# Performance work log

Hardware: AMD Instinct MI355X
Metric: run time of the kernel (lower is better)

The kernel has to match this reference:

```python
import jax, jax.numpy as jnp
import numpy as np

N_VERTICES = 1_000_000
N_EDGES = 16_000_000


def setup_inputs() -> dict:
    key = jax.random.key(0)
    k1, k2, k3 = jax.random.split(key, 3)
    vertex_attr = jax.random.normal(k1, (N_VERTICES, 2), dtype=jnp.float32)
    edgeij_pair = jax.random.randint(k2, (2, N_EDGES), 0, N_VERTICES, dtype=jnp.int64)
    edge_attr = jax.random.normal(k3, (N_EDGES, 2), dtype=jnp.float32)
    g = jnp.zeros((1, 1), dtype=jnp.float32)
    batch = jnp.zeros((N_VERTICES,), dtype=jnp.int64)
    return {"vertex_attr": vertex_attr, "edgeij_pair": edgeij_pair,
            "edge_attr": edge_attr, "g": g, "batch": batch}


def reference(vertex_attr, edgeij_pair, edge_attr, g, batch):
    # c_ij: second edge feature column, [E, 1]
    c_ij = edge_attr[:, 1:2]
    b_i = vertex_attr[:, 0:1]  # [N, 1]
    x_i = vertex_attr[:, 1:2]  # [N, 1]
    n_vertices = x_i.shape[0]
    # edge-to-vertex aggregation: sum c_ij into receiving vertex i (row 0)
    cbar_i = jax.ops.segment_sum(c_ij, edgeij_pair[0], num_segments=n_vertices)
    r_i = b_i - cbar_i
    return jnp.concatenate([b_i, x_i, r_i], axis=1)  # [N, 3]
```

## Files before the change

kernel.cpp:

```cpp
#include <hip/hip_runtime.h>


#define BSHIFT 11
#define BSIZE (1 << BSHIFT)
#define NBUCK_PAD 512
#define TILE 8192
#define TPB 1024

__global__ __launch_bounds__(TPB, 8)
void vu_partition(const int* __restrict__ src,
                  const float* __restrict__ eattr,
                  unsigned long long* __restrict__ pairs,
                  unsigned int* __restrict__ alloc,
                  int ne, int nbuck, int cap) {
    __shared__ unsigned long long sorted[TILE];
    __shared__ unsigned int hist[NBUCK_PAD];
    __shared__ unsigned int base_l[NBUCK_PAD];
    __shared__ unsigned int cursor[NBUCK_PAD];
    __shared__ unsigned int gbase[NBUCK_PAD];
    __shared__ unsigned int wsum[8];
    __shared__ unsigned int wexcl[8];

    int t = threadIdx.x;
    int tile0 = blockIdx.x * TILE;
    int lim = ne - tile0; if (lim > TILE) lim = TILE;
    bool full = (lim == TILE);

    if (t < NBUCK_PAD) hist[t] = 0u;
    __syncthreads();

    int4 sA, sB;
    float4 cA0, cA1, cB0, cB1;
    if (full) {
        const int4* s4 = (const int4*)(src + tile0);
        sA = s4[t];
        sB = s4[t + TPB];
        const float4* ef = (const float4*)eattr;
        int b0 = (tile0 >> 1) + 2 * t;
        cA0 = ef[b0];
        cA1 = ef[b0 + 1];
        cB0 = ef[b0 + 2048];
        cB1 = ef[b0 + 2049];
        atomicAdd(&hist[((unsigned)sA.x) >> BSHIFT], 1u);
        atomicAdd(&hist[((unsigned)sA.y) >> BSHIFT], 1u);
        atomicAdd(&hist[((unsigned)sA.z) >> BSHIFT], 1u);
        atomicAdd(&hist[((unsigned)sA.w) >> BSHIFT], 1u);
        atomicAdd(&hist[((unsigned)sB.x) >> BSHIFT], 1u);
        atomicAdd(&hist[((unsigned)sB.y) >> BSHIFT], 1u);
        atomicAdd(&hist[((unsigned)sB.z) >> BSHIFT], 1u);
        atomicAdd(&hist[((unsigned)sB.w) >> BSHIFT], 1u);
    } else {
        for (int i = t; i < lim; i += TPB)
            atomicAdd(&hist[((unsigned)src[tile0 + i]) >> BSHIFT], 1u);
    }
    __syncthreads();

    unsigned int mycnt = (t < NBUCK_PAD) ? hist[t] : 0u;
    unsigned int x = mycnt;
    #pragma unroll
    for (int off = 1; off < 64; off <<= 1) {
        unsigned int v = __shfl_up(x, off, 64);
        if ((t & 63) >= off) x += v;
    }
    if (t < NBUCK_PAD && (t & 63) == 63) wsum[t >> 6] = x;
    __syncthreads();
    if (t < 8) {
        unsigned int s = 0u;
        for (int k = 0; k < t; ++k) s += wsum[k];
        wexcl[t] = s;
    }
    __syncthreads();
    if (t < NBUCK_PAD) {
        unsigned int inc = x + wexcl[t >> 6];
        unsigned int excl = inc - mycnt;
        base_l[t] = excl;
        cursor[t] = excl;
        gbase[t] = (t < nbuck && mycnt) ? atomicAdd(&alloc[t], mycnt) : 0u;
    }
    __syncthreads();

#define VU_SCAT(sv, cv) do { \
        unsigned int q_ = ((unsigned)(sv)) >> BSHIFT; \
        unsigned int pos_ = atomicAdd(&cursor[q_], 1u); \
        sorted[pos_] = ((unsigned long long)__float_as_uint(cv) << 32) \
                       | (unsigned)(sv); } while (0)
    if (full) {
        VU_SCAT(sA.x, cA0.y); VU_SCAT(sA.y, cA0.w);
        VU_SCAT(sA.z, cA1.y); VU_SCAT(sA.w, cA1.w);
        VU_SCAT(sB.x, cB0.y); VU_SCAT(sB.y, cB0.w);
        VU_SCAT(sB.z, cB1.y); VU_SCAT(sB.w, cB1.w);
    } else {
        for (int i = t; i < lim; i += TPB) {
            int e = tile0 + i;
            int s = src[e];
            float2 ec = ((const float2*)eattr)[e];
            VU_SCAT(s, ec.y);
        }
    }
#undef VU_SCAT
    __syncthreads();

    for (int i = t; i < lim; i += TPB) {
        unsigned long long p = sorted[i];
        unsigned int q = ((unsigned int)p) >> BSHIFT;
        unsigned int dst = q * (unsigned int)cap + gbase[q]
                         + ((unsigned int)i - base_l[q]);
        unsigned int hi = q * (unsigned int)cap + (unsigned int)cap - 1u;
        if (dst > hi) dst = hi;
        pairs[dst] = p;
    }
}

__global__ __launch_bounds__(1024)
void vu_aggregate(const unsigned long long* __restrict__ pairs,
                  const unsigned int* __restrict__ alloc,
                  const float* __restrict__ vattr,
                  float* __restrict__ out,
                  int nv, int cap) {
    __shared__ float acc[BSIZE];
    __shared__ float obuf[BSIZE * 3];
    int q = blockIdx.x;
    int t = threadIdx.x;
    acc[t] = 0.0f;
    acc[t + 1024] = 0.0f;

    int v0 = q << BSHIFT;
    int iv0 = v0 + t, iv1 = v0 + t + 1024;
    float2 va0 = make_float2(0.f, 0.f), va1 = make_float2(0.f, 0.f);
    if (iv0 < nv) va0 = ((const float2*)vattr)[iv0];
    if (iv1 < nv) va1 = ((const float2*)vattr)[iv1];
    __syncthreads();

    unsigned int cnt = alloc[q];
    if (cnt > (unsigned int)cap) cnt = (unsigned int)cap;
    const unsigned long long* p = pairs + (size_t)q * (size_t)cap;
    const ulonglong2* p2 = (const ulonglong2*)p;
    unsigned int n2 = cnt >> 1;

#define VU_ACC(v64) do { \
        atomicAdd(&acc[((unsigned int)(v64)) & (BSIZE - 1)], \
                  __uint_as_float((unsigned int)((v64) >> 32))); } while (0)

    unsigned int i = t;
    for (; i + 3u * 1024u < n2; i += 4096u) {
        ulonglong2 v0 = p2[i];
        ulonglong2 v1 = p2[i + 1024u];
        ulonglong2 v2 = p2[i + 2048u];
        ulonglong2 v3 = p2[i + 3072u];
        VU_ACC(v0.x); VU_ACC(v0.y);
        VU_ACC(v1.x); VU_ACC(v1.y);
        VU_ACC(v2.x); VU_ACC(v2.y);
        VU_ACC(v3.x); VU_ACC(v3.y);
    }
    for (; i < n2; i += 1024u) {
        ulonglong2 v = p2[i];
        VU_ACC(v.x); VU_ACC(v.y);
    }
    if (t == 0 && (cnt & 1u)) {
        unsigned long long v = p[cnt - 1];
        VU_ACC(v);
    }
#undef VU_ACC
    __syncthreads();

    if (iv0 < nv) {
        obuf[3 * t + 0] = va0.x;
        obuf[3 * t + 1] = va0.y;
        obuf[3 * t + 2] = va0.x - acc[t];
    }
    {
        int i2 = t + 1024;
        if (iv1 < nv) {
            obuf[3 * i2 + 0] = va1.x;
            obuf[3 * i2 + 1] = va1.y;
            obuf[3 * i2 + 2] = va1.x - acc[i2];
        }
    }
    __syncthreads();

    long fbase = (long)q * (BSIZE * 3);
    int nfl = 3 * nv - (int)fbase;
    if (nfl > BSIZE * 3) nfl = BSIZE * 3;
    if (nfl > 0) {
        float4* o4 = (float4*)(out + fbase);
        const float4* s4 = (const float4*)obuf;
        int n4 = nfl >> 2;
        for (int j = t; j < n4; j += 1024) o4[j] = s4[j];
        for (int j = (n4 << 2) + t; j < nfl; j += 1024) out[fbase + j] = obuf[j];
    }
}

__global__ void vu_init_kernel(const float* __restrict__ vattr,
                               float* __restrict__ out, int n) {
    int i = blockIdx.x * blockDim.x + threadIdx.x;
    if (i < n) {
        float2 v = ((const float2*)vattr)[i];
        out[3 * i + 0] = v.x;
        out[3 * i + 1] = v.y;
        out[3 * i + 2] = v.x;
    }
}

__global__ void vu_scatter_kernel(const int* __restrict__ src,
                                  const float* __restrict__ eattr,
                                  float* __restrict__ out, int ne) {
    int t = blockIdx.x * blockDim.x + threadIdx.x;
    int e0 = t * 4;
    if (e0 + 3 < ne) {
        int4 idx = ((const int4*)src)[t];
        float4 a = ((const float4*)eattr)[2 * t + 0];
        float4 b = ((const float4*)eattr)[2 * t + 1];
        atomicAdd(&out[3 * idx.x + 2], -a.y);
        atomicAdd(&out[3 * idx.y + 2], -a.w);
        atomicAdd(&out[3 * idx.z + 2], -b.y);
        atomicAdd(&out[3 * idx.w + 2], -b.w);
    } else {
        for (int e = e0; e < ne; ++e)
            atomicAdd(&out[3 * src[e] + 2], -eattr[2 * e + 1]);
    }
}

extern "C" void kernel_launch(void* const* d_in, const int* in_sizes, int n_in,
                              void* d_out, int out_size, void* d_ws, size_t ws_size,
                              hipStream_t stream) {
    const float* vattr = (const float*)d_in[0];
    const int* edges = (const int*)d_in[1];
    const float* eattr = (const float*)d_in[2];
    float* out = (float*)d_out;

    int nv = in_sizes[0] / 2;
    int ne = in_sizes[2] / 2;

    int nbuck = (nv + BSIZE - 1) >> BSHIFT;
    int mean = ne / nbuck;
    int cap = mean + mean / 8 + 1024;
    cap = (cap + 15) & ~15;

    size_t alloc_bytes = 4096;
    size_t pair_bytes = (size_t)nbuck * (size_t)cap * 8ull;
    size_t need = alloc_bytes + pair_bytes;

    if (ws_size >= need && nbuck <= NBUCK_PAD) {
        unsigned int* alloc = (unsigned int*)d_ws;
        unsigned long long* pairs = (unsigned long long*)((char*)d_ws + alloc_bytes);
        (void)hipMemsetAsync(alloc, 0, (size_t)nbuck * 4, stream);

        int p1_blocks = (ne + TILE - 1) / TILE;
        vu_partition<<<p1_blocks, TPB, 0, stream>>>(edges, eattr, pairs, alloc,
                                                    ne, nbuck, cap);
        vu_aggregate<<<nbuck, 1024, 0, stream>>>(pairs, alloc, vattr, out, nv, cap);
    } else {
        int threads = 256;
        int blocks = (nv + threads - 1) / threads;
        vu_init_kernel<<<blocks, threads, 0, stream>>>(vattr, out, nv);
        int nt = (ne + 3) / 4;
        blocks = (nt + threads - 1) / threads;
        vu_scatter_kernel<<<blocks, threads, 0, stream>>>(edges, eattr, out, ne);
    }
}
```

Before: 390.3 us.

## Make partition kernel persistent with register prefetch of next tile

The partition kernel now runs as a fixed grid of persistent blocks that loop over edge tiles. Each iteration loads the next tile's source indices and edge values into registers before working on the current tile, so global load latency overlaps the LDS histogram, scan and scatter work. A custom barrier waits only on LDS counters, so the outstanding global prefetches are not drained at each barrier. The vector loads become strided scalar loads, and the extra registers could lower occupancy.

```diff
diff --git a/kernel.cpp b/kernel.cpp
--- a/kernel.cpp
+++ b/kernel.cpp
@@ -6,6 +6,11 @@
 #define NBUCK_PAD 512
 #define TILE 8192
 #define TPB 1024
+#define PGRID 512
+
+#define BARL() do { \
+    asm volatile("s_waitcnt lgkmcnt(0)" ::: "memory"); \
+    __builtin_amdgcn_s_barrier(); } while (0)
 
 __global__ __launch_bounds__(TPB, 8)
 void vu_partition(const int* __restrict__ src,
@@ -21,93 +26,132 @@
     __shared__ unsigned int wsum[8];
     __shared__ unsigned int wexcl[8];
 
-    int t = threadIdx.x;
-    int tile0 = blockIdx.x * TILE;
-    int lim = ne - tile0; if (lim > TILE) lim = TILE;
-    bool full = (lim == TILE);
-
+    const int t = threadIdx.x;
+    const int nt_tiles = (ne + TILE - 1) / TILE;
+
+    int   s0, s1, s2, s3, s4, s5, s6, s7;
+    float c0, c1, c2, c3, c4, c5, c6, c7;
+
+    int tk = blockIdx.x;
+
+    if (tk < nt_tiles) {
+        int tile0 = tk * TILE;
+        if (tile0 + TILE <= ne) {
+            const int* sp = src + tile0 + t;
+            const float* cp = eattr + 2 * (tile0 + t) + 1;
+            s0 = sp[0 * 1024]; s1 = sp[1 * 1024];
+            s2 = sp[2 * 1024]; s3 = sp[3 * 1024];
+            s4 = sp[4 * 1024]; s5 = sp[5 * 1024];
+            s6 = sp[6 * 1024]; s7 = sp[7 * 1024];
+            c0 = cp[0 * 2048]; c1 = cp[1 * 2048];
+            c2 = cp[2 * 2048]; c3 = cp[3 * 2048];
+            c4 = cp[4 * 2048]; c5 = cp[5 * 2048];
+            c6 = cp[6 * 2048]; c7 = cp[7 * 2048];
+        }
+    }
     if (t < NBUCK_PAD) hist[t] = 0u;
-    __syncthreads();
-
-    int4 sA, sB;
-    float4 cA0, cA1, cB0, cB1;
-    if (full) {
-        const int4* s4 = (const int4*)(src + tile0);
-        sA = s4[t];
-        sB = s4[t + TPB];
-        const float4* ef = (const float4*)eattr;
-        int b0 = (tile0 >> 1) + 2 * t;
-        cA0 = ef[b0];
-        cA1 = ef[b0 + 1];
-        cB0 = ef[b0 + 2048];
-        cB1 = ef[b0 + 2049];
-        atomicAdd(&hist[((unsigned)sA.x) >> BSHIFT], 1u);
-        atomicAdd(&hist[((unsigned)sA.y) >> BSHIFT], 1u);
-        atomicAdd(&hist[((unsigned)sA.z) >> BSHIFT], 1u);
-        atomicAdd(&hist[((unsigned)sA.w) >> BSHIFT], 1u);
-        atomicAdd(&hist[((unsigned)sB.x) >> BSHIFT], 1u);
-        atomicAdd(&hist[((unsigned)sB.y) >> BSHIFT], 1u);
-        atomicAdd(&hist[((unsigned)sB.z) >> BSHIFT], 1u);
-        atomicAdd(&hist[((unsigned)sB.w) >> BSHIFT], 1u);
-    } else {
-        for (int i = t; i < lim; i += TPB)
-            atomicAdd(&hist[((unsigned)src[tile0 + i]) >> BSHIFT], 1u);
-    }
-    __syncthreads();
-
-    unsigned int mycnt = (t < NBUCK_PAD) ? hist[t] : 0u;
-    unsigned int x = mycnt;
-    #pragma unroll
-    for (int off = 1; off < 64; off <<= 1) {
-        unsigned int v = __shfl_up(x, off, 64);
-        if ((t & 63) >= off) x += v;
-    }
-    if (t < NBUCK_PAD && (t & 63) == 63) wsum[t >> 6] = x;
-    __syncthreads();
-    if (t < 8) {
-        unsigned int s = 0u;
-        for (int k = 0; k < t; ++k) s += wsum[k];
-        wexcl[t] = s;
-    }
-    __syncthreads();
-    if (t < NBUCK_PAD) {
-        unsigned int inc = x + wexcl[t >> 6];
-        unsigned int excl = inc - mycnt;
-        base_l[t] = excl;
-        cursor[t] = excl;
-        gbase[t] = (t < nbuck && mycnt) ? atomicAdd(&alloc[t], mycnt) : 0u;
-    }
-    __syncthreads();
+    BARL();
+
+    for (; tk < nt_tiles; tk += PGRID) {
+        int tile0 = tk * TILE;
+        int lim = ne - tile0; if (lim > TILE) lim = TILE;
+        bool full = (lim == TILE);
+
+        int nk = tk + PGRID;
+        bool pv = (nk < nt_tiles) && (nk * TILE + TILE <= ne);
+        int   p0s, p1s, p2s, p3s, p4s, p5s, p6s, p7s;
+        float p0c, p1c, p2c, p3c, p4c, p5c, p6c, p7c;
+        if (pv) {
+            int ptile0 = nk * TILE;
+            const int* sp = src + ptile0 + t;
+            const float* cp = eattr + 2 * (ptile0 + t) + 1;
+            p0s = sp[0 * 1024]; p1s = sp[1 * 1024];
+            p2s = sp[2 * 1024]; p3s = sp[3 * 1024];
+            p4s = sp[4 * 1024]; p5s = sp[5 * 1024];
+            p6s = sp[6 * 1024]; p7s = sp[7 * 1024];
+            p0c = cp[0 * 2048]; p1c = cp[1 * 2048];
+            p2c = cp[2 * 2048]; p3c = cp[3 * 2048];
+            p4c = cp[4 * 2048]; p5c = cp[5 * 2048];
+            p6c = cp[6 * 2048]; p7c = cp[7 * 2048];
+        }
+
+        if (full) {
+            atomicAdd(&hist[((unsigned)s0) >> BSHIFT], 1u);
+            atomicAdd(&hist[((unsigned)s1) >> BSHIFT], 1u);
+            atomicAdd(&hist[((unsigned)s2) >> BSHIFT], 1u);
+            atomicAdd(&hist[((unsigned)s3) >> BSHIFT], 1u);
+            atomicAdd(&hist[((unsigned)s4) >> BSHIFT], 1u);
+            atomicAdd(&hist[((unsigned)s5) >> BSHIFT], 1u);
+            atomicAdd(&hist[((unsigned)s6) >> BSHIFT], 1u);
+            atomicAdd(&hist[((unsigned)s7) >> BSHIFT], 1u);
+        } else {
+            for (int i = t; i < lim; i += TPB)
+                atomicAdd(&hist[((unsigned)src[tile0 + i]) >> BSHIFT], 1u);
+        }
+        BARL();
+
+        unsigned int mycnt = (t < NBUCK_PAD) ? hist[t] : 0u;
+        if (t < NBUCK_PAD) hist[t] = 0u;
+        unsigned int gb = 0u;
+        if (t < nbuck && mycnt) gb = atomicAdd(&alloc[t], mycnt);
+
+        unsigned int x = mycnt;
+        #pragma unroll
+        for (int off = 1; off < 64; off <<= 1) {
+            unsigned int v = __shfl_up(x, off, 64);
+            if ((t & 63) >= off) x += v;
+        }
+        if (t < NBUCK_PAD && (t & 63) == 63) wsum[t >> 6] = x;
+        BARL();
+        if (t < 8) {
+            unsigned int s = 0u;
+            for (int k = 0; k < t; ++k) s += wsum[k];
+            wexcl[t] = s;
+        }
+        BARL();
+        if (t < NBUCK_PAD) {
+            unsigned int excl = x + wexcl[t >> 6] - mycnt;
+            base_l[t] = excl;
+            cursor[t] = excl;
+            gbase[t] = gb;
+        }
+        BARL();
 
 #define VU_SCAT(sv, cv) do { \
         unsigned int q_ = ((unsigned)(sv)) >> BSHIFT; \
         unsigned int pos_ = atomicAdd(&cursor[q_], 1u); \
         sorted[pos_] = ((unsigned long long)__float_as_uint(cv) << 32) \
                        | (unsigned)(sv); } while (0)
-    if (full) {
-        VU_SCAT(sA.x, cA0.y); VU_SCAT(sA.y, cA0.w);
-        VU_SCAT(sA.z, cA1.y); VU_SCAT(sA.w, cA1.w);
-        VU_SCAT(sB.x, cB0.y); VU_SCAT(sB.y, cB0.w);
-        VU_SCAT(sB.z, cB1.y); VU_SCAT(sB.w, cB1.w);
-    } else {
+        if (full) {
+            VU_SCAT(s0, c0); VU_SCAT(s1, c1);
+            VU_SCAT(s2, c2); VU_SCAT(s3, c3);
+            VU_SCAT(s4, c4); VU_SCAT(s5, c5);
+            VU_SCAT(s6, c6); VU_SCAT(s7, c7);
+        } else {
+            for (int i = t; i < lim; i += TPB) {
+                int e = tile0 + i;
+                int s = src[e];
+                float2 ec = ((const float2*)eattr)[e];
+                VU_SCAT(s, ec.y);
+            }
+        }
+#undef VU_SCAT
+        BARL();
+
         for (int i = t; i < lim; i += TPB) {
-            int e = tile0 + i;
-            int s = src[e];
-            float2 ec = ((const float2*)eattr)[e];
-            VU_SCAT(s, ec.y);
-        }
-    }
-#undef VU_SCAT
-    __syncthreads();
-
-    for (int i = t; i < lim; i += TPB) {
-        unsigned long long p = sorted[i];
-        unsigned int q = ((unsigned int)p) >> BSHIFT;
-        unsigned int dst = q * (unsigned int)cap + gbase[q]
-                         + ((unsigned int)i - base_l[q]);
-        unsigned int hi = q * (unsigned int)cap + (unsigned int)cap - 1u;
-        if (dst > hi) dst = hi;
-        pairs[dst] = p;
+            unsigned long long p = sorted[i];
+            unsigned int q = ((unsigned int)p) >> BSHIFT;
+            unsigned int dst = q * (unsigned int)cap + gbase[q]
+                             + ((unsigned int)i - base_l[q]);
+            unsigned int hi = q * (unsigned int)cap + (unsigned int)cap - 1u;
+            if (dst > hi) dst = hi;
+            pairs[dst] = p;
+        }
+
+        s0 = p0s; s1 = p1s; s2 = p2s; s3 = p3s;
+        s4 = p4s; s5 = p5s; s6 = p6s; s7 = p7s;
+        c0 = p0c; c1 = p1c; c2 = p2c; c3 = p3c;
+        c4 = p4c; c5 = p5c; c6 = p6c; c7 = p7c;
     }
 }
 
@@ -245,9 +289,10 @@
         unsigned long long* pairs = (unsigned long long*)((char*)d_ws + alloc_bytes);
         (void)hipMemsetAsync(alloc, 0, (size_t)nbuck * 4, stream);
 
-        int p1_blocks = (ne + TILE - 1) / TILE;
-        vu_partition<<<p1_blocks, TPB, 0, stream>>>(edges, eattr, pairs, alloc,
-                                                    ne, nbuck, cap);
+        int nt_tiles = (ne + TILE - 1) / TILE;
+        int grid = PGRID; if (grid > nt_tiles) grid = nt_tiles;
+        vu_partition<<<grid, TPB, 0, stream>>>(edges, eattr, pairs, alloc,
+                                               ne, nbuck, cap);
         vu_aggregate<<<nbuck, 1024, 0, stream>>>(pairs, alloc, vattr, out, nv, cap);
     } else {
         int threads = 256;
```

Result: no change. 396.9 us (+1.7%).
